# Optimization experiments

Measured on AMD Instinct MI355X. Metric: run time of the kernel, lower is better.

## Reference

```python
import jax, jax.numpy as jnp
import numpy as np

S_D, I_D, O_D = 512, 256, 256
BATCH, T = 64, 1024
SNR = 10.0  # noise scale divisor, as in sample_stable_system
SPECTRAL_RADIUS = 0.95  # stable F, mirroring sample_stable_state_matrix


def setup_inputs() -> dict:
    key = jax.random.key(0)
    ks = jax.random.split(key, 9)
    A = np.asarray(jax.random.normal(ks[0], (S_D, S_D), dtype=jnp.float32))
    F = jnp.asarray(A * (SPECTRAL_RADIUS / np.linalg.norm(A, 2)))  # scale to spectral norm 0.95
    B_mat = jax.random.normal(ks[1], (S_D, I_D), dtype=jnp.float32)
    H = jax.random.normal(ks[2], (O_D, S_D), dtype=jnp.float32)
    sqrt_S_W = jax.random.normal(ks[3], (S_D, S_D), dtype=jnp.float32) / SNR
    sqrt_S_V = jax.random.normal(ks[4], (O_D, O_D), dtype=jnp.float32) / SNR
    state = jax.random.normal(ks[5], (BATCH, S_D), dtype=jnp.float32)
    inputs = jax.random.normal(ks[6], (BATCH, T, I_D), dtype=jnp.float32)
    W_noise = jax.random.normal(ks[7], (BATCH, T, S_D), dtype=jnp.float32)
    V_noise = jax.random.normal(ks[8], (BATCH, T, O_D), dtype=jnp.float32)
    return {"state": state, "inputs": inputs, "W_noise": W_noise, "V_noise": V_noise,
            "F": F, "B_mat": B_mat, "H": H, "sqrt_S_W": sqrt_S_W, "sqrt_S_V": sqrt_S_V}


def reference(state, inputs, W_noise, V_noise, F, B_mat, H, sqrt_S_W, sqrt_S_V):
    # Process noise W = eps_W @ sqrt_S_W.T, measurement noise V = eps_V @ sqrt_S_V.T
    W = jnp.einsum('bti,ji->btj', W_noise, sqrt_S_W)          # (B, T, S_D)
    V = jnp.einsum('bti,ji->btj', V_noise, sqrt_S_V)          # (B, T, O_D)
    drive = jnp.einsum('bti,ji->btj', inputs, B_mat) + W      # u_t @ B.T + W_t

    def step(s, u):  # s_t = s_{t-1} @ F.T + u_t
        s = s @ F.T + u
        return s, s

    _, states_t = jax.lax.scan(step, state, jnp.swapaxes(drive, 0, 1))  # (T, B, S_D)
    states = jnp.swapaxes(states_t, 0, 1)                                # (B, T, S_D)
    observations = jnp.einsum('bts,os->bto', states, H) + V              # (B, T, O_D)
    return states, observations
```

## Files before the change

kernel.cpp:

```cpp
#include <hip/hip_runtime.h>
#include <hip/hip_bf16.h>


typedef short bfrag __attribute__((ext_vector_type(8)));
typedef float f32x4 __attribute__((ext_vector_type(4)));

__device__ __host__ inline unsigned short f2bf(float f) {
    union { float f; unsigned u; } x; x.f = f;
    unsigned r = x.u + 0x7fffu + ((x.u >> 16) & 1u);
    return (unsigned short)(r >> 16);
}
__device__ inline float bf2f(unsigned short h) {
    union { unsigned u; float f; } x; x.u = ((unsigned)h) << 16;
    return x.f;
}

#define MSL 262144L

struct GemmDesc {
    const void* a0; const void* a1;
    const unsigned short* b;
    float* c;
    const unsigned short* cmbeta;
    unsigned short* cm;
    unsigned short* cmT;
    long a0_base, a0_os, a0_is;
    long a1_base, a1_os, a1_is;
    long a_zq, a_zr;
    long b_base, b_ldb, b_zq, b_zr;
    long c_base, c_os, c_is, c_zq, c_zr;
    long cm_base, cmb_base, cmT_base;
    long a_shift;
    int a0_icl, a1_icl, c_icl, zdivl;
    int ksplit, K, beta;
    int a0_f32, a1_f32;
    int gxl, gyl, gz_main;
    const unsigned short* xa; const unsigned short* xb;
    unsigned short* xcm; unsigned short* xcmT;
};

__global__ __launch_bounds__(256) void gemm_k(GemmDesc d) {
    __shared__ __align__(16) unsigned short As[2][128 * 64];
    __shared__ __align__(16) unsigned short Bs[2][128 * 64];
    const int tid  = threadIdx.x;
    const int lane = tid & 63;
    const int w    = tid >> 6;
    const int wrow = (w >> 1) * 64, wcol = (w & 1) * 64;

    const unsigned nx = gridDim.x, ny = gridDim.y;
    const unsigned nwg = nx * ny * gridDim.z;
    unsigned wid = blockIdx.x + nx * (blockIdx.y + ny * blockIdx.z);
    if ((nwg & 7) == 0) wid = (wid & 7) * (nwg >> 3) + (wid >> 3);
    const int bx = wid & (nx - 1);
    const int by = (wid >> d.gxl) & (ny - 1);
    int bz = wid >> (d.gxl + d.gyl);

    if (bz >= d.gz_main) {
        if (by >= 4) return;
        const long za = (long)(bz - d.gz_main) * MSL;
        d.a0 = d.xa; d.a0_base = za; d.a0_os = 512; d.a0_is = 0; d.a0_icl = 0;
        d.a0_f32 = 0; d.a1 = nullptr;
        d.b = d.xb; d.b_base = 0; d.b_ldb = 512; d.b_zq = d.b_zr = 0;
        d.K = 512; d.ksplit = 1 << 30; d.beta = 0; d.a_shift = 0;
        d.a_zq = d.a_zr = 0;
        d.c = nullptr; d.cm = d.xcm; d.cm_base = za;
        d.c_os = 512; d.c_is = 0; d.c_icl = 0; d.c_zq = d.c_zr = 0; d.c_base = 0;
        d.cmT = d.xcmT; d.cmT_base = za;
        bz = 0;
    }
    const long zq = (long)bz >> d.zdivl;
    const long zr = (long)bz & ((1L << d.zdivl) - 1);
    const int row0 = by * 128;
    const int col0 = bx * 128;

    const int g_r = tid >> 3;
    const int g_k = (tid & 7) * 8;
    const int swz = (g_r & 7) << 3;
    const long za_ = zq * d.a_zq + zr * d.a_zr;
    const long zb_ = zq * d.b_zq + zr * d.b_zr;

    const long m0a = (1L << d.a0_icl) - 1, m1a = (1L << d.a1_icl) - 1;
    long a0off[4], a1off[4], boff[4];
#pragma unroll
    for (int i = 0; i < 4; ++i) {
        long ar = (long)row0 + i * 32 + g_r - d.a_shift;
        if (ar < 0) ar = 0;
        a0off[i] = d.a0_base + za_ + (ar >> d.a0_icl) * d.a0_os + (ar & m0a) * d.a0_is;
        a1off[i] = d.a1 ? (d.a1_base + za_ + (ar >> d.a1_icl) * d.a1_os + (ar & m1a) * d.a1_is) : 0;
        boff[i]  = d.b_base + zb_ + (long)(col0 + i * 32 + g_r) * d.b_ldb;
    }

    bfrag ar_[4], br_[4];
    auto LOADT = [&](int t) {
        const int k0 = t * 64;
        const bool s1 = (k0 >= d.ksplit);
        const int kb = (s1 ? k0 - d.ksplit : k0) + g_k;
        if (s1 ? d.a1_f32 : d.a0_f32) {
            const float* fp = (const float*)(s1 ? d.a1 : d.a0);
#pragma unroll
            for (int i = 0; i < 4; ++i) {
                const float* p = fp + (s1 ? a1off[i] : a0off[i]) + kb;
                f32x4 x0 = *(const f32x4*)p, x1 = *(const f32x4*)(p + 4);
                union { bfrag v; unsigned short h[8]; } t_;
#pragma unroll
                for (int q = 0; q < 4; ++q) { t_.h[q] = f2bf(x0[q]); t_.h[4 + q] = f2bf(x1[q]); }
                ar_[i] = t_.v;
            }
        } else {
            const unsigned short* sp = (const unsigned short*)(s1 ? d.a1 : d.a0);
#pragma unroll
            for (int i = 0; i < 4; ++i)
                ar_[i] = *(const bfrag*)(sp + (s1 ? a1off[i] : a0off[i]) + kb);
        }
#pragma unroll
        for (int i = 0; i < 4; ++i) br_[i] = *(const bfrag*)(d.b + boff[i] + k0 + g_k);
    };
    auto WRT = [&](int buf) {
#pragma unroll
        for (int i = 0; i < 4; ++i) {
            *(bfrag*)&As[buf][(i * 32 + g_r) * 64 + (g_k ^ swz)] = ar_[i];
            *(bfrag*)&Bs[buf][(i * 32 + g_r) * 64 + (g_k ^ swz)] = br_[i];
        }
    };

    f32x4 acc[4][4] = {};
    const int nt = d.K / 64;

    LOADT(0); WRT(0); __syncthreads();
    int cur = 0;
    for (int t = 0; t < nt; ++t) {
        if (t + 1 < nt) LOADT(t + 1);
#pragma unroll
        for (int ks = 0; ks < 2; ++ks) {
            const int kk = ks * 32 + (lane >> 4) * 8;
            bfrag af[4], bf_[4];
#pragma unroll
            for (int mt = 0; mt < 4; ++mt) {
                const int r = wrow + mt * 16 + (lane & 15);
                af[mt] = *(const bfrag*)&As[cur][r * 64 + (kk ^ ((r & 7) << 3))];
            }
#pragma unroll
            for (int nn = 0; nn < 4; ++nn) {
                const int r = wcol + nn * 16 + (lane & 15);
                bf_[nn] = *(const bfrag*)&Bs[cur][r * 64 + (kk ^ ((r & 7) << 3))];
            }
#pragma unroll
            for (int mt = 0; mt < 4; ++mt)
#pragma unroll
                for (int nn = 0; nn < 4; ++nn)
                    acc[mt][nn] = __builtin_amdgcn_mfma_f32_16x16x32_bf16(
                        af[mt], bf_[nn], acc[mt][nn], 0, 0, 0);
        }
        if (t + 1 < nt) WRT(cur ^ 1);
        __syncthreads();
        cur ^= 1;
    }

    const long zc = zq * d.c_zq + zr * d.c_zr;
    const long mc = (1L << d.c_icl) - 1;
#pragma unroll
    for (int mt = 0; mt < 4; ++mt) {
        const int rb = row0 + wrow + mt * 16 + ((lane >> 4) << 2);
#pragma unroll
        for (int nn = 0; nn < 4; ++nn) {
            const int cc = col0 + wcol + nn * 16 + (lane & 15);
#pragma unroll
            for (int j = 0; j < 4; ++j) {
                const long r = rb + j;
                const long off = zc + (r >> d.c_icl) * d.c_os + (r & mc) * d.c_is + cc;
                float v = (r < d.a_shift) ? 0.0f : acc[mt][nn][j];
                if (d.beta == 2) v += bf2f(d.cmbeta[d.cmb_base + off]);
                if (d.c)  d.c[d.c_base + off] = v;
                if (d.cm) d.cm[d.cm_base + off] = f2bf(v);
                if (d.cmT) d.cmT[d.cmT_base + zc + (long)cc * 512 + r] = f2bf(v);
            }
        }
    }
}

__global__ __launch_bounds__(512) void p3obs_k(
        const unsigned short* __restrict__ carry, const unsigned short* __restrict__ Gm,
        const unsigned short* __restrict__ Smir, const unsigned short* __restrict__ BopO,
        const float* __restrict__ Vn, float* __restrict__ states, float* __restrict__ obs) {
    __shared__ __align__(16) unsigned char lds[163840];
    unsigned short* As1 = (unsigned short*)(lds);
    unsigned short* Bs1 = (unsigned short*)(lds + 16384);
    unsigned short* Sb  = (unsigned short*)(lds);
    unsigned short* A2  = (unsigned short*)(lds);
    unsigned short* Ts  = (unsigned short*)(lds + 131072);

    const int tid  = threadIdx.x;
    const int lane = tid & 63;
    const int w    = tid >> 6;
    const int wm   = w >> 2, wn = w & 3;
    const int by   = blockIdx.y;
    const int k    = blockIdx.z;
    const unsigned short* G = Gm + (long)k * MSL;

    f32x4 acc[4][8] = {};

    for (int kt = 0; kt < 8; ++kt) {
        __syncthreads();
#pragma unroll
        for (int i = 0; i < 2; ++i) {
            const int fi = tid + i * 512;
            const int row = fi >> 3, kk = (fi & 7) * 8;
            const long rg = (long)by * 128 + row;
            const long c = rg >> 6, b = rg & 63;
            bfrag v = *(const bfrag*)(carry + c * 32768 + b * 512 + kt * 64 + kk);
            *(bfrag*)&As1[row * 64 + (kk ^ ((row & 7) << 3))] = v;
        }
#pragma unroll
        for (int i = 0; i < 8; ++i) {
            const int fi = tid + i * 512;
            const int row = fi >> 3, kk = (fi & 7) * 8;
            bfrag v = *(const bfrag*)(G + (long)row * 512 + kt * 64 + kk);
            *(bfrag*)&Bs1[row * 64 + (kk ^ ((row & 7) << 3))] = v;
        }
        __syncthreads();
#pragma unroll
        for (int ks = 0; ks < 2; ++ks) {
            const int kk = ks * 32 + (lane >> 4) * 8;
            bfrag af[4], bf_[8];
#pragma unroll
            for (int mt = 0; mt < 4; ++mt) {
                const int r = wm * 64 + mt * 16 + (lane & 15);
                af[mt] = *(const bfrag*)&As1[r * 64 + (kk ^ ((r & 7) << 3))];
            }
#pragma unroll
            for (int nt = 0; nt < 8; ++nt) {
                const int n = wn * 128 + nt * 16 + (lane & 15);
                bf_[nt] = *(const bfrag*)&Bs1[n * 64 + (kk ^ ((n & 7) << 3))];
            }
#pragma unroll
            for (int mt = 0; mt < 4; ++mt)
#pragma unroll
                for (int nt = 0; nt < 8; ++nt)
                    acc[mt][nt] = __builtin_amdgcn_mfma_f32_16x16x32_bf16(
                        af[mt], bf_[nt], acc[mt][nt], 0, 0, 0);
        }
    }
    __syncthreads();

#pragma unroll
    for (int mt = 0; mt < 4; ++mt) {
#pragma unroll
        for (int nt = 0; nt < 8; ++nt) {
#pragma unroll
            for (int j = 0; j < 4; ++j) {
                const int lr = wm * 64 + mt * 16 + ((lane >> 4) << 2) + j;
                const int cc = wn * 128 + nt * 16 + (lane & 15);
                const long rg = (long)by * 128 + lr;
                const long c = rg >> 6, b = rg & 63;
                const long t = c * 8 + k;
                float v = acc[mt][nt][j] + bf2f(Smir[b * 524288L + t * 512 + cc]);
                states[b * 524288L + t * 512 + cc] = v;
                Sb[lr * 512 + (cc ^ ((lr & 7) << 3))] = f2bf(v);
            }
        }
    }

    f32x4 acc2[4][4] = {};
    for (int kt = 0; kt < 12; ++kt) {
        __syncthreads();
#pragma unroll
        for (int i = 0; i < 4; ++i) {
            const int fi = tid + i * 512;
            const int row = fi >> 3, kk = (fi & 7) * 8;
            bfrag v = *(const bfrag*)(BopO + (long)row * 768 + kt * 64 + kk);
            *(bfrag*)&Ts[row * 64 + (kk ^ ((row & 7) << 3))] = v;
        }
        if (kt >= 8) {
#pragma unroll
            for (int i = 0; i < 2; ++i) {
                const int fi = tid + i * 512;
                const int row = fi >> 3, kk = (fi & 7) * 8;
                const long rg = (long)by * 128 + row;
                const long c = rg >> 6, b = rg & 63;
                const long t = c * 8 + k;
                const float* p = Vn + b * 262144L + t * 256 + (kt - 8) * 64 + kk;
                f32x4 x0 = *(const f32x4*)p, x1 = *(const f32x4*)(p + 4);
                union { bfrag v; unsigned short h[8]; } u;
#pragma unroll
                for (int q = 0; q < 4; ++q) { u.h[q] = f2bf(x0[q]); u.h[4 + q] = f2bf(x1[q]); }
                *(bfrag*)&A2[row * 64 + (kk ^ ((row & 7) << 3))] = u.v;
            }
        }
        __syncthreads();
#pragma unroll
        for (int ks = 0; ks < 2; ++ks) {
            const int kk = ks * 32 + (lane >> 4) * 8;
            bfrag af[4], bf_[4];
#pragma unroll
            for (int mt = 0; mt < 4; ++mt) {
                const int r = wm * 64 + mt * 16 + (lane & 15);
                af[mt] = (kt < 8)
                    ? *(const bfrag*)&Sb[r * 512 + ((kt * 64 + kk) ^ ((r & 7) << 3))]
                    : *(const bfrag*)&A2[r * 64 + (kk ^ ((r & 7) << 3))];
            }
#pragma unroll
            for (int nt = 0; nt < 4; ++nt) {
                const int n = wn * 64 + nt * 16 + (lane & 15);
                bf_[nt] = *(const bfrag*)&Ts[n * 64 + (kk ^ ((n & 7) << 3))];
            }
#pragma unroll
            for (int mt = 0; mt < 4; ++mt)
#pragma unroll
                for (int nt = 0; nt < 4; ++nt)
                    acc2[mt][nt] = __builtin_amdgcn_mfma_f32_16x16x32_bf16(
                        af[mt], bf_[nt], acc2[mt][nt], 0, 0, 0);
        }
    }
#pragma unroll
    for (int mt = 0; mt < 4; ++mt) {
#pragma unroll
        for (int nt = 0; nt < 4; ++nt) {
#pragma unroll
            for (int j = 0; j < 4; ++j) {
                const int lr = wm * 64 + mt * 16 + ((lane >> 4) << 2) + j;
                const int cc = wn * 64 + nt * 16 + (lane & 15);
                const long rg = (long)by * 128 + lr;
                const long c = rg >> 6, b = rg & 63;
                const long t = c * 8 + k;
                obs[b * 262144L + t * 256 + cc] = acc2[mt][nt][j];
            }
        }
    }
}

__global__ void cvt_k(const float* src, unsigned short* dst, long n) {
    long i = ((long)blockIdx.x * 256 + threadIdx.x) * 8;
    const long stride = (long)gridDim.x * 256 * 8;
    for (; i < n; i += stride) {
        f32x4 x0 = *(const f32x4*)(src + i), x1 = *(const f32x4*)(src + i + 4);
        union { bfrag v; unsigned short h[8]; } t;
#pragma unroll
        for (int q = 0; q < 4; ++q) { t.h[q] = f2bf(x0[q]); t.h[4 + q] = f2bf(x1[q]); }
        *(bfrag*)(dst + i) = t.v;
    }
}

__global__ void build_ops_k(const float* F, const float* Bm, const float* H,
                            const float* sW, const float* sV,
                            unsigned short* bopd, unsigned short* bopo,
                            unsigned short* G1, unsigned short* Gt1) {
    int i = blockIdx.x * 256 + threadIdx.x;
    const int n1 = 512 * 768, n2 = 256 * 768, n3 = 512 * 512;
    if (i < n1) { int n = i / 768, k = i % 768;
        bopd[i] = f2bf(k < 256 ? Bm[n * 256 + k] : sW[n * 512 + (k - 256)]); return; }
    i -= n1;
    if (i < n2) { int o = i / 768, k = i % 768;
        bopo[i] = f2bf(k < 512 ? H[o * 512 + k] : sV[o * 256 + (k - 512)]); return; }
    i -= n2;
    if (i < n3) { G1[i] = f2bf(F[i]); return; }
    i -= n3;
    if (i < n3) { int r = i / 512, c = i % 512; Gt1[i] = f2bf(F[c * 512 + r]); }
}

__global__ void init_carry_k(const float* st0, const unsigned short* Smir,
                             unsigned short* dst) {
    const long i8 = ((long)blockIdx.x * 256 + threadIdx.x) * 8;
    if (i8 >= 4194304L) return;
    const long c = i8 >> 15, rem = i8 & 32767L;
    const long b = rem >> 9, s = rem & 511L;
    union { bfrag v; unsigned short h[8]; } t;
    if (c == 0) {
        const float* p = st0 + b * 512 + s;
        f32x4 x0 = *(const f32x4*)p, x1 = *(const f32x4*)(p + 4);
#pragma unroll
        for (int q = 0; q < 4; ++q) { t.h[q] = f2bf(x0[q]); t.h[4 + q] = f2bf(x1[q]); }
    } else {
        t.v = *(const bfrag*)(Smir + b * 524288L + (c - 1) * 4096L + 3584L + s);
    }
    *(bfrag*)(dst + i8) = t.v;
}

static GemmDesc D0() {
    GemmDesc d = {};
    d.zdivl = 30;
    d.ksplit = 1 << 30;
    d.b_ldb = 512; d.K = 512;
    d.gz_main = 1 << 30;
    return d;
}

extern "C" void kernel_launch(void* const* d_in, const int* in_sizes, int n_in,
                              void* d_out, int out_size, void* d_ws, size_t ws_size,
                              hipStream_t stream) {
    const float* st0 = (const float*)d_in[0];
    const float* inp = (const float*)d_in[1];
    const float* Wn  = (const float*)d_in[2];
    const float* Vn  = (const float*)d_in[3];
    const float* F   = (const float*)d_in[4];
    const float* Bm  = (const float*)d_in[5];
    const float* H   = (const float*)d_in[6];
    const float* sW  = (const float*)d_in[7];
    const float* sV  = (const float*)d_in[8];

    float* states = (float*)d_out;
    float* obs    = states + 33554432L;

    const long MS = MSL;
    const long CB = 32768;
    const int  NC = 128;
    const int  CL = 8;
    const long TOS = 524288;
    const long COS = (long)CL * 512;

    unsigned short* inpb = (unsigned short*)states;
    unsigned short* Wnb  = inpb + 16777216L;

    unsigned short* Smir = (unsigned short*)d_ws;
    unsigned short* G    = Smir + 33554432L;
    unsigned short* Gt   = G + 8 * MS;
    unsigned short* Qb   = Gt + 8 * MS;
    unsigned short* Qtb  = Qb + 6 * MS;
    unsigned short* BopD = Qtb + 6 * MS;
    unsigned short* BopO = BopD + 512 * 768;
    unsigned short* a0m  = BopO + 256 * 768;
    unsigned short* a1m  = a0m + (long)NC * CB;
    (void)in_sizes; (void)n_in; (void)out_size; (void)ws_size;

    auto L = [&](const GemmDesc& d, int gx, int gxl, int gy, int gyl, int gz) {
        GemmDesc dd = d; dd.gxl = gxl; dd.gyl = gyl;
        gemm_k<<<dim3(gx, gy, gz), dim3(256), 0, stream>>>(dd);
    };

    cvt_k<<<dim3(2048), dim3(256), 0, stream>>>(inp, inpb, 16777216L);
    cvt_k<<<dim3(2048), dim3(256), 0, stream>>>(Wn, Wnb, 33554432L);

    build_ops_k<<<dim3(4352), dim3(256), 0, stream>>>(F, Bm, H, sW, sV, BopD, BopO, G, Gt);

    {
        GemmDesc d = D0();
        d.a0 = inpb; d.a0_os = 256;
        d.a1 = Wnb;  d.a1_os = 512;
        d.ksplit = 256; d.K = 768;
        d.b = BopD; d.b_ldb = 768;
        d.cm = Smir; d.c_os = 512;
        L(d, 4, 2, 512, 9, 1);
    }

    for (int k = 1; k < CL; ++k) {
        GemmDesc d = D0();
        d.a0 = Smir; d.a0_base = (long)(k - 1) * 512;
        d.a0_icl = 7; d.a0_is = COS; d.a0_os = TOS;
        d.b = G;
        d.c_base = (long)k * 512;
        d.c_icl = 7; d.c_is = COS; d.c_os = TOS;
        d.beta = 2; d.cmbeta = Smir; d.cmb_base = (long)k * 512;
        d.cm = Smir; d.cm_base = (long)k * 512;
        d.gz_main = 1;
        int n;
        if (k == 1)      { d.xa = G;           d.xb = Gt;           d.xcm = G + MS;      d.xcmT = Gt + MS;      n = 1; }
        else if (k == 2) { d.xa = G;           d.xb = Gt + MS;      d.xcm = G + 2 * MS;  d.xcmT = Gt + 2 * MS;  n = 2; }
        else if (k == 3) { d.xa = G;           d.xb = Gt + 3 * MS;  d.xcm = G + 4 * MS;  d.xcmT = Gt + 4 * MS;  n = 4; }
        else if (k == 4) { d.xa = G + 7 * MS;  d.xb = Gt + 7 * MS;  d.xcm = Qb;          d.xcmT = Qtb;          n = 1; }
        else             { int j = k - 5;
                           d.xa = Qb + j * MS; d.xb = Qtb + j * MS; d.xcm = Qb + (j+1)*MS; d.xcmT = Qtb + (j+1)*MS; n = 1; }
        L(d, 4, 2, 64, 6, 1 + n);
    }

    init_carry_k<<<dim3(2048), dim3(256), 0, stream>>>(st0, Smir, a0m);

    unsigned short* curm = a0m;
    unsigned short* nxtm = a1m;
    for (int s = 1; s < NC; s <<= 1) {
        GemmDesc d = D0();
        d.a0 = curm; d.a0_os = 512;
        d.a_shift = (long)s * 64;
        if (s == 1) { d.b = G;  d.b_base = 7 * MS; }
        else        { d.b = Qb; d.b_base = (long)(__builtin_ctz(s) - 1) * MS; }
        d.beta = 2; d.cmbeta = curm; d.cmb_base = 0;
        d.cm = nxtm; d.c_os = 512;
        int n = 0;
        if (s == 1) { d.gz_main = 1; d.xa = Qb + 3 * MS; d.xb = Qtb + 3 * MS;
                      d.xcm = Qb + 4 * MS; d.xcmT = Qtb + 4 * MS; n = 1; }
        if (s == 2) { d.gz_main = 1; d.xa = Qb + 4 * MS; d.xb = Qtb + 4 * MS;
                      d.xcm = Qb + 5 * MS; d.xcmT = nullptr; n = 1; }
        L(d, 4, 2, 64, 6, 1 + n);
        unsigned short* tm = curm; curm = nxtm; nxtm = tm;
    }

    p3obs_k<<<dim3(1, 64, 8), dim3(512), 0, stream>>>(
        curm, G, Smir, BopO, Vn, states, obs);
}
```

Before: 703.7 us.

## Restructure intra-chunk scan into log-depth passes and double-buffer observation kernel

Replaces the seven sequential intra-chunk propagation GEMMs with three doubling passes (shifts 1, 2, 4). Each pass uses ping-pong buffers plus auxiliary copy blocks, and the G-power computations are folded into existing launches, including the first drive GEMM. The observation kernel gets register-staged double-buffered LDS loads to overlap global loads with MFMA, and its grid is reordered so the chunk index is on x. The f32 A-path is removed from the GEMM. The goal is fewer serialized launches and less load latency, at the cost of more total GEMM work and extra copy traffic through the states buffer.

Result: slower. 940.6 us (+33.7%).

```diff
diff --git a/kernel.cpp b/kernel.cpp
--- a/kernel.cpp
+++ b/kernel.cpp
@@ -18,12 +18,13 @@
 #define MSL 262144L
 
 struct GemmDesc {
-    const void* a0; const void* a1;
+    const unsigned short* a0;
     const unsigned short* b;
     float* c;
     const unsigned short* cmbeta;
     unsigned short* cm;
     unsigned short* cmT;
+    const unsigned short* a1;
     long a0_base, a0_os, a0_is;
     long a1_base, a1_os, a1_is;
     long a_zq, a_zr;
@@ -33,8 +34,8 @@
     long a_shift;
     int a0_icl, a1_icl, c_icl, zdivl;
     int ksplit, K, beta;
-    int a0_f32, a1_f32;
-    int gxl, gyl, gz_main;
+    int gxl, gyl, gz_main, gz_ncp;
+    const unsigned short* cp_src; unsigned short* cp_dst; long cp_nrows;
     const unsigned short* xa; const unsigned short* xb;
     unsigned short* xcm; unsigned short* xcmT;
 };
@@ -56,10 +57,22 @@
     int bz = wid >> (d.gxl + d.gyl);
 
     if (bz >= d.gz_main) {
+        const int aux_z = bz - d.gz_main - d.gz_ncp;
+        if (aux_z < 0) {
+            const long total = (long)nx * ny * 256;
+            const long flatb = wid & (nx * ny - 1);
+            for (long i8 = (flatb * 256 + tid) * 8; i8 < d.cp_nrows * 512; i8 += total * 8) {
+                const long r = i8 >> 9, s = i8 & 511;
+                const long t = r >> 13, q = r & 8191;
+                const long off = (q >> 7) * 524288L + (q & 127) * 4096L + t * 512L + s;
+                *(bfrag*)(d.cp_dst + off) = *(const bfrag*)(d.cp_src + off);
+            }
+            return;
+        }
         if (by >= 4) return;
-        const long za = (long)(bz - d.gz_main) * MSL;
+        const long za = (long)aux_z * MSL;
         d.a0 = d.xa; d.a0_base = za; d.a0_os = 512; d.a0_is = 0; d.a0_icl = 0;
-        d.a0_f32 = 0; d.a1 = nullptr;
+        d.a1 = nullptr;
         d.b = d.xb; d.b_base = 0; d.b_ldb = 512; d.b_zq = d.b_zr = 0;
         d.K = 512; d.ksplit = 1 << 30; d.beta = 0; d.a_shift = 0;
         d.a_zq = d.a_zr = 0;
@@ -95,23 +108,10 @@
         const int k0 = t * 64;
         const bool s1 = (k0 >= d.ksplit);
         const int kb = (s1 ? k0 - d.ksplit : k0) + g_k;
-        if (s1 ? d.a1_f32 : d.a0_f32) {
-            const float* fp = (const float*)(s1 ? d.a1 : d.a0);
-#pragma unroll
-            for (int i = 0; i < 4; ++i) {
-                const float* p = fp + (s1 ? a1off[i] : a0off[i]) + kb;
-                f32x4 x0 = *(const f32x4*)p, x1 = *(const f32x4*)(p + 4);
-                union { bfrag v; unsigned short h[8]; } t_;
-#pragma unroll
-                for (int q = 0; q < 4; ++q) { t_.h[q] = f2bf(x0[q]); t_.h[4 + q] = f2bf(x1[q]); }
-                ar_[i] = t_.v;
-            }
-        } else {
-            const unsigned short* sp = (const unsigned short*)(s1 ? d.a1 : d.a0);
-#pragma unroll
-            for (int i = 0; i < 4; ++i)
-                ar_[i] = *(const bfrag*)(sp + (s1 ? a1off[i] : a0off[i]) + kb);
-        }
+        const unsigned short* sp = s1 ? d.a1 : d.a0;
+#pragma unroll
+        for (int i = 0; i < 4; ++i)
+            ar_[i] = *(const bfrag*)(sp + (s1 ? a1off[i] : a0off[i]) + kb);
 #pragma unroll
         for (int i = 0; i < 4; ++i) br_[i] = *(const bfrag*)(d.b + boff[i] + k0 + g_k);
     };
@@ -183,41 +183,54 @@
         const unsigned short* __restrict__ Smir, const unsigned short* __restrict__ BopO,
         const float* __restrict__ Vn, float* __restrict__ states, float* __restrict__ obs) {
     __shared__ __align__(16) unsigned char lds[163840];
-    unsigned short* As1 = (unsigned short*)(lds);
-    unsigned short* Bs1 = (unsigned short*)(lds + 16384);
-    unsigned short* Sb  = (unsigned short*)(lds);
-    unsigned short* A2  = (unsigned short*)(lds);
-    unsigned short* Ts  = (unsigned short*)(lds + 131072);
+#define BS1(buf) ((unsigned short*)(lds + (buf) * 65536))
+#define AS1(buf) ((unsigned short*)(lds + 131072 + (buf) * 16384))
+    unsigned short* Sb = (unsigned short*)lds;
+    unsigned short* Ts = (unsigned short*)(lds + 131072);
+    unsigned short* A2 = (unsigned short*)lds;
 
     const int tid  = threadIdx.x;
     const int lane = tid & 63;
     const int w    = tid >> 6;
     const int wm   = w >> 2, wn = w & 3;
+    const int k    = blockIdx.x;
     const int by   = blockIdx.y;
-    const int k    = blockIdx.z;
     const unsigned short* G = Gm + (long)k * MSL;
 
+    const int srow = tid >> 3;
+    const int skk  = (tid & 7) * 8;
+    const int sw   = (srow & 7) << 3;
+
+    bfrag areg[2], breg[8];
+    auto LOADT = [&](int kt) {
+#pragma unroll
+        for (int i = 0; i < 2; ++i) {
+            const int row = srow + i * 64;
+            const long rg = (long)by * 128 + row;
+            areg[i] = *(const bfrag*)(carry + (rg >> 6) * 32768 + (rg & 63) * 512 + kt * 64 + skk);
+        }
+#pragma unroll
+        for (int i = 0; i < 8; ++i)
+            breg[i] = *(const bfrag*)(G + (long)(srow + i * 64) * 512 + kt * 64 + skk);
+    };
+    auto WRT = [&](int buf) {
+        unsigned short* as = AS1(buf);
+        unsigned short* bs = BS1(buf);
+#pragma unroll
+        for (int i = 0; i < 2; ++i)
+            *(bfrag*)&as[(srow + i * 64) * 64 + (skk ^ sw)] = areg[i];
+#pragma unroll
+        for (int i = 0; i < 8; ++i)
+            *(bfrag*)&bs[(srow + i * 64) * 64 + (skk ^ sw)] = breg[i];
+    };
+
     f32x4 acc[4][8] = {};
-
+    LOADT(0); WRT(0); __syncthreads();
+    int cur = 0;
     for (int kt = 0; kt < 8; ++kt) {
-        __syncthreads();
-#pragma unroll
-        for (int i = 0; i < 2; ++i) {
-            const int fi = tid + i * 512;
-            const int row = fi >> 3, kk = (fi & 7) * 8;
-            const long rg = (long)by * 128 + row;
-            const long c = rg >> 6, b = rg & 63;
-            bfrag v = *(const bfrag*)(carry + c * 32768 + b * 512 + kt * 64 + kk);
-            *(bfrag*)&As1[row * 64 + (kk ^ ((row & 7) << 3))] = v;
-        }
-#pragma unroll
-        for (int i = 0; i < 8; ++i) {
-            const int fi = tid + i * 512;
-            const int row = fi >> 3, kk = (fi & 7) * 8;
-            bfrag v = *(const bfrag*)(G + (long)row * 512 + kt * 64 + kk);
-            *(bfrag*)&Bs1[row * 64 + (kk ^ ((row & 7) << 3))] = v;
-        }
-        __syncthreads();
+        if (kt < 7) LOADT(kt + 1);
+        const unsigned short* as = AS1(cur);
+        const unsigned short* bs = BS1(cur);
 #pragma unroll
         for (int ks = 0; ks < 2; ++ks) {
             const int kk = ks * 32 + (lane >> 4) * 8;
@@ -225,12 +238,12 @@
 #pragma unroll
             for (int mt = 0; mt < 4; ++mt) {
                 const int r = wm * 64 + mt * 16 + (lane & 15);
-                af[mt] = *(const bfrag*)&As1[r * 64 + (kk ^ ((r & 7) << 3))];
+                af[mt] = *(const bfrag*)&as[r * 64 + (kk ^ ((r & 7) << 3))];
             }
 #pragma unroll
             for (int nt = 0; nt < 8; ++nt) {
                 const int n = wn * 128 + nt * 16 + (lane & 15);
-                bf_[nt] = *(const bfrag*)&Bs1[n * 64 + (kk ^ ((n & 7) << 3))];
+                bf_[nt] = *(const bfrag*)&bs[n * 64 + (kk ^ ((n & 7) << 3))];
             }
 #pragma unroll
             for (int mt = 0; mt < 4; ++mt)
@@ -239,8 +252,10 @@
                     acc[mt][nt] = __builtin_amdgcn_mfma_f32_16x16x32_bf16(
                         af[mt], bf_[nt], acc[mt][nt], 0, 0, 0);
         }
-    }
-    __syncthreads();
+        if (kt < 7) WRT(cur ^ 1);
+        __syncthreads();
+        cur ^= 1;
+    }
 
 #pragma unroll
     for (int mt = 0; mt < 4; ++mt) {
@@ -251,8 +266,8 @@
                 const int lr = wm * 64 + mt * 16 + ((lane >> 4) << 2) + j;
                 const int cc = wn * 128 + nt * 16 + (lane & 15);
                 const long rg = (long)by * 128 + lr;
-                const long c = rg >> 6, b = rg & 63;
-                const long t = c * 8 + k;
+                const long b = rg & 63;
+                const long t = (rg >> 6) * 8 + k;
                 float v = acc[mt][nt][j] + bf2f(Smir[b * 524288L + t * 512 + cc]);
                 states[b * 524288L + t * 512 + cc] = v;
                 Sb[lr * 512 + (cc ^ ((lr & 7) << 3))] = f2bf(v);
@@ -276,8 +291,8 @@
                 const int fi = tid + i * 512;
                 const int row = fi >> 3, kk = (fi & 7) * 8;
                 const long rg = (long)by * 128 + row;
-                const long c = rg >> 6, b = rg & 63;
-                const long t = c * 8 + k;
+                const long b = rg & 63;
+                const long t = (rg >> 6) * 8 + k;
                 const float* p = Vn + b * 262144L + t * 256 + (kt - 8) * 64 + kk;
                 f32x4 x0 = *(const f32x4*)p, x1 = *(const f32x4*)(p + 4);
                 union { bfrag v; unsigned short h[8]; } u;
@@ -320,12 +335,14 @@
                 const int lr = wm * 64 + mt * 16 + ((lane >> 4) << 2) + j;
                 const int cc = wn * 64 + nt * 16 + (lane & 15);
                 const long rg = (long)by * 128 + lr;
-                const long c = rg >> 6, b = rg & 63;
-                const long t = c * 8 + k;
+                const long b = rg & 63;
+                const long t = (rg >> 6) * 8 + k;
                 obs[b * 262144L + t * 256 + cc] = acc2[mt][nt][j];
             }
         }
     }
+#undef BS1
+#undef AS1
 }
 
 __global__ void cvt_k(const float* src, unsigned short* dst, long n) {
@@ -403,12 +420,12 @@
     const long MS = MSL;
     const long CB = 32768;
     const int  NC = 128;
-    const int  CL = 8;
     const long TOS = 524288;
-    const long COS = (long)CL * 512;
+    const long COS = 4096;
 
     unsigned short* inpb = (unsigned short*)states;
     unsigned short* Wnb  = inpb + 16777216L;
+    unsigned short* BufA = (unsigned short*)states;
 
     unsigned short* Smir = (unsigned short*)d_ws;
     unsigned short* G    = Smir + 33554432L;
@@ -438,50 +455,72 @@
         d.ksplit = 256; d.K = 768;
         d.b = BopD; d.b_ldb = 768;
         d.cm = Smir; d.c_os = 512;
-        L(d, 4, 2, 512, 9, 1);
-    }
-
-    for (int k = 1; k < CL; ++k) {
+        d.gz_main = 1;
+        d.xa = G; d.xb = Gt; d.xcm = G + MS; d.xcmT = Gt + MS;
+        L(d, 4, 2, 512, 9, 2);
+    }
+
+    {
         GemmDesc d = D0();
-        d.a0 = Smir; d.a0_base = (long)(k - 1) * 512;
-        d.a0_icl = 7; d.a0_is = COS; d.a0_os = TOS;
+        d.a0 = Smir; d.a0_icl = 7; d.a0_os = TOS; d.a0_is = COS; d.a_zr = 512;
         d.b = G;
-        d.c_base = (long)k * 512;
-        d.c_icl = 7; d.c_is = COS; d.c_os = TOS;
-        d.beta = 2; d.cmbeta = Smir; d.cmb_base = (long)k * 512;
-        d.cm = Smir; d.cm_base = (long)k * 512;
-        d.gz_main = 1;
-        int n;
-        if (k == 1)      { d.xa = G;           d.xb = Gt;           d.xcm = G + MS;      d.xcmT = Gt + MS;      n = 1; }
-        else if (k == 2) { d.xa = G;           d.xb = Gt + MS;      d.xcm = G + 2 * MS;  d.xcmT = Gt + 2 * MS;  n = 2; }
-        else if (k == 3) { d.xa = G;           d.xb = Gt + 3 * MS;  d.xcm = G + 4 * MS;  d.xcmT = Gt + 4 * MS;  n = 4; }
-        else if (k == 4) { d.xa = G + 7 * MS;  d.xb = Gt + 7 * MS;  d.xcm = Qb;          d.xcmT = Qtb;          n = 1; }
-        else             { int j = k - 5;
-                           d.xa = Qb + j * MS; d.xb = Qtb + j * MS; d.xcm = Qb + (j+1)*MS; d.xcmT = Qtb + (j+1)*MS; n = 1; }
-        L(d, 4, 2, 64, 6, 1 + n);
+        d.cm = BufA; d.cm_base = 512;
+        d.c_icl = 7; d.c_os = TOS; d.c_is = COS; d.c_zr = 512;
+        d.beta = 2; d.cmbeta = Smir; d.cmb_base = 512;
+        d.gz_main = 7; d.gz_ncp = 1;
+        d.cp_src = Smir; d.cp_dst = BufA; d.cp_nrows = 8192;
+        d.xa = G; d.xb = Gt + MS; d.xcm = G + 2 * MS; d.xcmT = Gt + 2 * MS;
+        L(d, 4, 2, 64, 6, 10);
+    }
+    {
+        GemmDesc d = D0();
+        d.a0 = BufA; d.a0_icl = 7; d.a0_os = TOS; d.a0_is = COS; d.a_zr = 512;
+        d.b = G + MS;
+        d.cm = Smir; d.cm_base = 1024;
+        d.c_icl = 7; d.c_os = TOS; d.c_is = COS; d.c_zr = 512;
+        d.beta = 2; d.cmbeta = BufA; d.cmb_base = 1024;
+        d.gz_main = 6; d.gz_ncp = 1;
+        d.cp_src = BufA; d.cp_dst = Smir; d.cp_nrows = 16384;
+        d.xa = G; d.xb = Gt + 3 * MS; d.xcm = G + 4 * MS; d.xcmT = Gt + 4 * MS;
+        L(d, 4, 2, 64, 6, 11);
+    }
+    {
+        GemmDesc d = D0();
+        d.a0 = Smir; d.a0_icl = 7; d.a0_os = TOS; d.a0_is = COS; d.a_zr = 512;
+        d.b = G + 3 * MS;
+        d.cm = Smir; d.cm_base = 2048;
+        d.c_icl = 7; d.c_os = TOS; d.c_is = COS; d.c_zr = 512;
+        d.beta = 2; d.cmbeta = Smir; d.cmb_base = 2048;
+        d.gz_main = 4;
+        d.xa = G + 7 * MS; d.xb = Gt + 7 * MS; d.xcm = Qb; d.xcmT = Qtb;
+        L(d, 4, 2, 64, 6, 5);
     }
 
     init_carry_k<<<dim3(2048), dim3(256), 0, stream>>>(st0, Smir, a0m);
 
     unsigned short* curm = a0m;
     unsigned short* nxtm = a1m;
-    for (int s = 1; s < NC; s <<= 1) {
+    int ksi = 0;
+    for (int s = 1; s < NC; s <<= 1, ++ksi) {
         GemmDesc d = D0();
         d.a0 = curm; d.a0_os = 512;
         d.a_shift = (long)s * 64;
-        if (s == 1) { d.b = G;  d.b_base = 7 * MS; }
-        else        { d.b = Qb; d.b_base = (long)(__builtin_ctz(s) - 1) * MS; }
+        if (s == 1) { d.b = G + 7 * MS; }
+        else        { d.b = Qb + (long)(__builtin_ctz(s) - 1) * MS; }
         d.beta = 2; d.cmbeta = curm; d.cmb_base = 0;
         d.cm = nxtm; d.c_os = 512;
         int n = 0;
-        if (s == 1) { d.gz_main = 1; d.xa = Qb + 3 * MS; d.xb = Qtb + 3 * MS;
-                      d.xcm = Qb + 4 * MS; d.xcmT = Qtb + 4 * MS; n = 1; }
-        if (s == 2) { d.gz_main = 1; d.xa = Qb + 4 * MS; d.xb = Qtb + 4 * MS;
-                      d.xcm = Qb + 5 * MS; d.xcmT = nullptr; n = 1; }
+        if (ksi < 5) {
+            d.gz_main = 1;
+            d.xa = Qb + (long)ksi * MS; d.xb = Qtb + (long)ksi * MS;
+            d.xcm = Qb + (long)(ksi + 1) * MS;
+            d.xcmT = (ksi < 4) ? (Qtb + (long)(ksi + 1) * MS) : nullptr;
+            n = 1;
+        }
         L(d, 4, 2, 64, 6, 1 + n);
         unsigned short* tm = curm; curm = nxtm; nxtm = tm;
     }
 
-    p3obs_k<<<dim3(1, 64, 8), dim3(512), 0, stream>>>(
+    p3obs_k<<<dim3(8, 64, 1), dim3(512), 0, stream>>>(
         curm, G, Smir, BopO, Vn, states, obs);
 }
```

## Halve chunk length to four steps and double chunk count in scan

Applied to the files above, without the earlier changes.

Changes the chunked linear recurrence from 128 chunks of 8 steps to 256 chunks of 4 steps, reducing the number of sequential intra-chunk GEMM launches. The inter-chunk doubling scan gains an extra level over twice as many rows, and F-power precomputation is folded into the first drive GEMM launch. It also drops the unused fp32 A-load path from the GEMM kernel. This trades serial launch depth against more total work in the carry-propagation scan.

After: 867.9 us. 1.23x slower.

```diff
diff --git a/kernel.cpp b/kernel.cpp
--- a/kernel.cpp
+++ b/kernel.cpp
@@ -18,7 +18,7 @@
 #define MSL 262144L
 
 struct GemmDesc {
-    const void* a0; const void* a1;
+    const unsigned short* a0; const unsigned short* a1;
     const unsigned short* b;
     float* c;
     const unsigned short* cmbeta;
@@ -33,7 +33,6 @@
     long a_shift;
     int a0_icl, a1_icl, c_icl, zdivl;
     int ksplit, K, beta;
-    int a0_f32, a1_f32;
     int gxl, gyl, gz_main;
     const unsigned short* xa; const unsigned short* xb;
     unsigned short* xcm; unsigned short* xcmT;
@@ -59,7 +58,7 @@
         if (by >= 4) return;
         const long za = (long)(bz - d.gz_main) * MSL;
         d.a0 = d.xa; d.a0_base = za; d.a0_os = 512; d.a0_is = 0; d.a0_icl = 0;
-        d.a0_f32 = 0; d.a1 = nullptr;
+        d.a1 = nullptr;
         d.b = d.xb; d.b_base = 0; d.b_ldb = 512; d.b_zq = d.b_zr = 0;
         d.K = 512; d.ksplit = 1 << 30; d.beta = 0; d.a_shift = 0;
         d.a_zq = d.a_zr = 0;
@@ -95,23 +94,10 @@
         const int k0 = t * 64;
         const bool s1 = (k0 >= d.ksplit);
         const int kb = (s1 ? k0 - d.ksplit : k0) + g_k;
-        if (s1 ? d.a1_f32 : d.a0_f32) {
-            const float* fp = (const float*)(s1 ? d.a1 : d.a0);
-#pragma unroll
-            for (int i = 0; i < 4; ++i) {
-                const float* p = fp + (s1 ? a1off[i] : a0off[i]) + kb;
-                f32x4 x0 = *(const f32x4*)p, x1 = *(const f32x4*)(p + 4);
-                union { bfrag v; unsigned short h[8]; } t_;
-#pragma unroll
-                for (int q = 0; q < 4; ++q) { t_.h[q] = f2bf(x0[q]); t_.h[4 + q] = f2bf(x1[q]); }
-                ar_[i] = t_.v;
-            }
-        } else {
-            const unsigned short* sp = (const unsigned short*)(s1 ? d.a1 : d.a0);
-#pragma unroll
-            for (int i = 0; i < 4; ++i)
-                ar_[i] = *(const bfrag*)(sp + (s1 ? a1off[i] : a0off[i]) + kb);
-        }
+        const unsigned short* sp = s1 ? d.a1 : d.a0;
+#pragma unroll
+        for (int i = 0; i < 4; ++i)
+            ar_[i] = *(const bfrag*)(sp + (s1 ? a1off[i] : a0off[i]) + kb);
 #pragma unroll
         for (int i = 0; i < 4; ++i) br_[i] = *(const bfrag*)(d.b + boff[i] + k0 + g_k);
     };
@@ -252,7 +238,7 @@
                 const int cc = wn * 128 + nt * 16 + (lane & 15);
                 const long rg = (long)by * 128 + lr;
                 const long c = rg >> 6, b = rg & 63;
-                const long t = c * 8 + k;
+                const long t = c * 4 + k;
                 float v = acc[mt][nt][j] + bf2f(Smir[b * 524288L + t * 512 + cc]);
                 states[b * 524288L + t * 512 + cc] = v;
                 Sb[lr * 512 + (cc ^ ((lr & 7) << 3))] = f2bf(v);
@@ -277,7 +263,7 @@
                 const int row = fi >> 3, kk = (fi & 7) * 8;
                 const long rg = (long)by * 128 + row;
                 const long c = rg >> 6, b = rg & 63;
-                const long t = c * 8 + k;
+                const long t = c * 4 + k;
                 const float* p = Vn + b * 262144L + t * 256 + (kt - 8) * 64 + kk;
                 f32x4 x0 = *(const f32x4*)p, x1 = *(const f32x4*)(p + 4);
                 union { bfrag v; unsigned short h[8]; } u;
@@ -321,7 +307,7 @@
                 const int cc = wn * 64 + nt * 16 + (lane & 15);
                 const long rg = (long)by * 128 + lr;
                 const long c = rg >> 6, b = rg & 63;
-                const long t = c * 8 + k;
+                const long t = c * 4 + k;
                 obs[b * 262144L + t * 256 + cc] = acc2[mt][nt][j];
             }
         }
@@ -360,7 +346,7 @@
 __global__ void init_carry_k(const float* st0, const unsigned short* Smir,
                              unsigned short* dst) {
     const long i8 = ((long)blockIdx.x * 256 + threadIdx.x) * 8;
-    if (i8 >= 4194304L) return;
+    if (i8 >= 8388608L) return;
     const long c = i8 >> 15, rem = i8 & 32767L;
     const long b = rem >> 9, s = rem & 511L;
     union { bfrag v; unsigned short h[8]; } t;
@@ -370,7 +356,7 @@
 #pragma unroll
         for (int q = 0; q < 4; ++q) { t.h[q] = f2bf(x0[q]); t.h[4 + q] = f2bf(x1[q]); }
     } else {
-        t.v = *(const bfrag*)(Smir + b * 524288L + (c - 1) * 4096L + 3584L + s);
+        t.v = *(const bfrag*)(Smir + b * 524288L + (c - 1) * 2048L + 1536L + s);
     }
     *(bfrag*)(dst + i8) = t.v;
 }
@@ -402,8 +388,8 @@
 
     const long MS = MSL;
     const long CB = 32768;
-    const int  NC = 128;
-    const int  CL = 8;
+    const int  NC = 256;
+    const int  CL = 4;
     const long TOS = 524288;
     const long COS = (long)CL * 512;
 
@@ -412,9 +398,9 @@
 
     unsigned short* Smir = (unsigned short*)d_ws;
     unsigned short* G    = Smir + 33554432L;
-    unsigned short* Gt   = G + 8 * MS;
-    unsigned short* Qb   = Gt + 8 * MS;
-    unsigned short* Qtb  = Qb + 6 * MS;
+    unsigned short* Gt   = G + 4 * MS;
+    unsigned short* Qb   = Gt + 4 * MS;
+    unsigned short* Qtb  = Qb + 7 * MS;
     unsigned short* BopD = Qtb + 6 * MS;
     unsigned short* BopO = BopD + 512 * 768;
     unsigned short* a0m  = BopO + 256 * 768;
@@ -438,50 +424,53 @@
         d.ksplit = 256; d.K = 768;
         d.b = BopD; d.b_ldb = 768;
         d.cm = Smir; d.c_os = 512;
-        L(d, 4, 2, 512, 9, 1);
+        d.gz_main = 1;
+        d.xa = G; d.xb = Gt; d.xcm = G + MS; d.xcmT = Gt + MS;
+        L(d, 4, 2, 512, 9, 2);
     }
 
     for (int k = 1; k < CL; ++k) {
         GemmDesc d = D0();
         d.a0 = Smir; d.a0_base = (long)(k - 1) * 512;
-        d.a0_icl = 7; d.a0_is = COS; d.a0_os = TOS;
+        d.a0_icl = 8; d.a0_is = COS; d.a0_os = TOS;
         d.b = G;
         d.c_base = (long)k * 512;
-        d.c_icl = 7; d.c_is = COS; d.c_os = TOS;
+        d.c_icl = 8; d.c_is = COS; d.c_os = TOS;
         d.beta = 2; d.cmbeta = Smir; d.cmb_base = (long)k * 512;
         d.cm = Smir; d.cm_base = (long)k * 512;
         d.gz_main = 1;
         int n;
-        if (k == 1)      { d.xa = G;           d.xb = Gt;           d.xcm = G + MS;      d.xcmT = Gt + MS;      n = 1; }
-        else if (k == 2) { d.xa = G;           d.xb = Gt + MS;      d.xcm = G + 2 * MS;  d.xcmT = Gt + 2 * MS;  n = 2; }
-        else if (k == 3) { d.xa = G;           d.xb = Gt + 3 * MS;  d.xcm = G + 4 * MS;  d.xcmT = Gt + 4 * MS;  n = 4; }
-        else if (k == 4) { d.xa = G + 7 * MS;  d.xb = Gt + 7 * MS;  d.xcm = Qb;          d.xcmT = Qtb;          n = 1; }
-        else             { int j = k - 5;
-                           d.xa = Qb + j * MS; d.xb = Qtb + j * MS; d.xcm = Qb + (j+1)*MS; d.xcmT = Qtb + (j+1)*MS; n = 1; }
-        L(d, 4, 2, 64, 6, 1 + n);
-    }
-
-    init_carry_k<<<dim3(2048), dim3(256), 0, stream>>>(st0, Smir, a0m);
+        if (k == 1)      { d.xa = G;          d.xb = Gt + MS;     d.xcm = G + 2 * MS; d.xcmT = Gt + 2 * MS; n = 2; }
+        else if (k == 2) { d.xa = G + 3 * MS; d.xb = Gt + 3 * MS; d.xcm = Qb;         d.xcmT = Qtb;         n = 1; }
+        else             { d.xa = Qb;         d.xb = Qtb;         d.xcm = Qb + MS;    d.xcmT = Qtb + MS;    n = 1; }
+        L(d, 4, 2, 128, 7, 1 + n);
+    }
+
+    init_carry_k<<<dim3(4096), dim3(256), 0, stream>>>(st0, Smir, a0m);
 
     unsigned short* curm = a0m;
     unsigned short* nxtm = a1m;
-    for (int s = 1; s < NC; s <<= 1) {
+    int ri = 0;
+    for (int s = 1; s < NC; s <<= 1, ++ri) {
         GemmDesc d = D0();
         d.a0 = curm; d.a0_os = 512;
         d.a_shift = (long)s * 64;
-        if (s == 1) { d.b = G;  d.b_base = 7 * MS; }
-        else        { d.b = Qb; d.b_base = (long)(__builtin_ctz(s) - 1) * MS; }
+        if (s == 1) { d.b = G + 3 * MS; }
+        else        { d.b = Qb + (long)(__builtin_ctz(s) - 1) * MS; }
         d.beta = 2; d.cmbeta = curm; d.cmb_base = 0;
         d.cm = nxtm; d.c_os = 512;
         int n = 0;
-        if (s == 1) { d.gz_main = 1; d.xa = Qb + 3 * MS; d.xb = Qtb + 3 * MS;
-                      d.xcm = Qb + 4 * MS; d.xcmT = Qtb + 4 * MS; n = 1; }
-        if (s == 2) { d.gz_main = 1; d.xa = Qb + 4 * MS; d.xb = Qtb + 4 * MS;
-                      d.xcm = Qb + 5 * MS; d.xcmT = nullptr; n = 1; }
-        L(d, 4, 2, 64, 6, 1 + n);
+        if (ri < 5) {
+            d.gz_main = 1;
+            d.xa = Qb + (long)(ri + 1) * MS; d.xb = Qtb + (long)(ri + 1) * MS;
+            d.xcm = Qb + (long)(ri + 2) * MS;
+            d.xcmT = (ri < 4) ? (Qtb + (long)(ri + 2) * MS) : nullptr;
+            n = 1;
+        }
+        L(d, 4, 2, 128, 7, 1 + n);
         unsigned short* tm = curm; curm = nxtm; nxtm = tm;
     }
 
-    p3obs_k<<<dim3(1, 64, 8), dim3(512), 0, stream>>>(
+    p3obs_k<<<dim3(1, 128, 4), dim3(512), 0, stream>>>(
         curm, G, Smir, BopO, Vn, states, obs);
 }
```

## Replace intra-chunk scan GEMM launches with a persistent LDS-resident scan kernel

Applied to the files above, without the earlier changes.

Replaces the seven per-step intra-chunk GEMM launches with a single scan_k kernel. Each block keeps 32 chunk rows of the state in LDS and streams F tiles through double-buffered LDS for all 7 sequential steps. The power-of-F matrix products are regrouped: F^2, F^3 and F^4..F^7 are computed in separate small launches, and the later Q powers are folded into the carry-propagation rounds. This cuts launch count and global round trips of the state, but each scan block re-reads F from global memory for every step. The scan also runs on only 256 blocks, so occupancy is limited. The dead fp32 A-load path is removed from the GEMM kernel.

Result: slower. 828.0 us (+17.7%).

```diff
diff --git a/kernel.cpp b/kernel.cpp
--- a/kernel.cpp
+++ b/kernel.cpp
@@ -18,7 +18,7 @@
 #define MSL 262144L
 
 struct GemmDesc {
-    const void* a0; const void* a1;
+    const unsigned short* a0; const unsigned short* a1;
     const unsigned short* b;
     float* c;
     const unsigned short* cmbeta;
@@ -33,7 +33,6 @@
     long a_shift;
     int a0_icl, a1_icl, c_icl, zdivl;
     int ksplit, K, beta;
-    int a0_f32, a1_f32;
     int gxl, gyl, gz_main;
     const unsigned short* xa; const unsigned short* xb;
     unsigned short* xcm; unsigned short* xcmT;
@@ -59,7 +58,7 @@
         if (by >= 4) return;
         const long za = (long)(bz - d.gz_main) * MSL;
         d.a0 = d.xa; d.a0_base = za; d.a0_os = 512; d.a0_is = 0; d.a0_icl = 0;
-        d.a0_f32 = 0; d.a1 = nullptr;
+        d.a1 = nullptr;
         d.b = d.xb; d.b_base = 0; d.b_ldb = 512; d.b_zq = d.b_zr = 0;
         d.K = 512; d.ksplit = 1 << 30; d.beta = 0; d.a_shift = 0;
         d.a_zq = d.a_zr = 0;
@@ -95,23 +94,10 @@
         const int k0 = t * 64;
         const bool s1 = (k0 >= d.ksplit);
         const int kb = (s1 ? k0 - d.ksplit : k0) + g_k;
-        if (s1 ? d.a1_f32 : d.a0_f32) {
-            const float* fp = (const float*)(s1 ? d.a1 : d.a0);
-#pragma unroll
-            for (int i = 0; i < 4; ++i) {
-                const float* p = fp + (s1 ? a1off[i] : a0off[i]) + kb;
-                f32x4 x0 = *(const f32x4*)p, x1 = *(const f32x4*)(p + 4);
-                union { bfrag v; unsigned short h[8]; } t_;
-#pragma unroll
-                for (int q = 0; q < 4; ++q) { t_.h[q] = f2bf(x0[q]); t_.h[4 + q] = f2bf(x1[q]); }
-                ar_[i] = t_.v;
-            }
-        } else {
-            const unsigned short* sp = (const unsigned short*)(s1 ? d.a1 : d.a0);
-#pragma unroll
-            for (int i = 0; i < 4; ++i)
-                ar_[i] = *(const bfrag*)(sp + (s1 ? a1off[i] : a0off[i]) + kb);
-        }
+        const unsigned short* sp = s1 ? d.a1 : d.a0;
+#pragma unroll
+        for (int i = 0; i < 4; ++i)
+            ar_[i] = *(const bfrag*)(sp + (s1 ? a1off[i] : a0off[i]) + kb);
 #pragma unroll
         for (int i = 0; i < 4; ++i) br_[i] = *(const bfrag*)(d.b + boff[i] + k0 + g_k);
     };
@@ -175,6 +161,101 @@
                 if (d.cmT) d.cmT[d.cmT_base + zc + (long)cc * 512 + r] = f2bf(v);
             }
         }
+    }
+}
+
+__global__ __launch_bounds__(512) void scan_k(
+        unsigned short* __restrict__ Smir, const unsigned short* __restrict__ Fm) {
+    __shared__ __align__(16) unsigned char lds[163840];
+    unsigned short* Scur = (unsigned short*)lds;
+
+    const int tid  = threadIdx.x;
+    const int lane = tid & 63;
+    const int w    = tid >> 6;
+    const long rg0 = (long)blockIdx.x * 32;
+
+    const int fr = tid >> 3;
+    const int fk = (tid & 7) * 8;
+
+    bfrag freg[8];
+    auto LOADF = [&](int kt) {
+#pragma unroll
+        for (int i = 0; i < 8; ++i)
+            freg[i] = *(const bfrag*)(Fm + (long)(fr + i * 64) * 512 + kt * 64 + fk);
+    };
+    auto WRTF = [&](int buf) {
+        unsigned short* Fs = (unsigned short*)(lds + 32768 + buf * 65536);
+#pragma unroll
+        for (int i = 0; i < 8; ++i) {
+            const int r = fr + i * 64;
+            *(bfrag*)&Fs[r * 64 + (fk ^ ((r & 7) << 3))] = freg[i];
+        }
+    };
+
+#pragma unroll
+    for (int i = 0; i < 4; ++i) {
+        const int fi = tid + i * 512;
+        const int row = fi >> 6;
+        const int col = (fi & 63) * 8;
+        const long rg = rg0 + row;
+        const long b = rg >> 7, c = rg & 127;
+        bfrag v = *(const bfrag*)(Smir + b * 524288L + c * 4096L + col);
+        *(bfrag*)&Scur[row * 512 + (col ^ ((row & 7) << 3))] = v;
+    }
+    LOADF(0); WRTF(0);
+    __syncthreads();
+
+    int cur = 0;
+    for (int t = 1; t < 8; ++t) {
+        f32x4 acc[2][4] = {};
+        for (int kt = 0; kt < 8; ++kt) {
+            const bool pre = !(t == 7 && kt == 7);
+            if (pre) LOADF((kt + 1) & 7);
+            const unsigned short* Fs = (const unsigned short*)(lds + 32768 + cur * 65536);
+#pragma unroll
+            for (int ks = 0; ks < 2; ++ks) {
+                const int kk = ks * 32 + (lane >> 4) * 8;
+                bfrag af[2], bf_[4];
+#pragma unroll
+                for (int mt = 0; mt < 2; ++mt) {
+                    const int r = mt * 16 + (lane & 15);
+                    const int col = kt * 64 + kk;
+                    af[mt] = *(const bfrag*)&Scur[r * 512 + (col ^ ((r & 7) << 3))];
+                }
+#pragma unroll
+                for (int nt = 0; nt < 4; ++nt) {
+                    const int n = w * 64 + nt * 16 + (lane & 15);
+                    bf_[nt] = *(const bfrag*)&Fs[n * 64 + (kk ^ ((n & 7) << 3))];
+                }
+#pragma unroll
+                for (int mt = 0; mt < 2; ++mt)
+#pragma unroll
+                    for (int nt = 0; nt < 4; ++nt)
+                        acc[mt][nt] = __builtin_amdgcn_mfma_f32_16x16x32_bf16(
+                            af[mt], bf_[nt], acc[mt][nt], 0, 0, 0);
+            }
+            if (pre) WRTF(cur ^ 1);
+            __syncthreads();
+            cur ^= 1;
+        }
+#pragma unroll
+        for (int mt = 0; mt < 2; ++mt) {
+#pragma unroll
+            for (int nt = 0; nt < 4; ++nt) {
+#pragma unroll
+                for (int j = 0; j < 4; ++j) {
+                    const int lr = mt * 16 + ((lane >> 4) << 2) + j;
+                    const int cc = w * 64 + nt * 16 + (lane & 15);
+                    const long rg = rg0 + lr;
+                    const long b = rg >> 7, c = rg & 127;
+                    const long off = b * 524288L + c * 4096L + (long)t * 512 + cc;
+                    const unsigned short bv = f2bf(acc[mt][nt][j] + bf2f(Smir[off]));
+                    Smir[off] = bv;
+                    Scur[lr * 512 + (cc ^ ((lr & 7) << 3))] = bv;
+                }
+            }
+        }
+        __syncthreads();
     }
 }
 
@@ -403,9 +484,6 @@
     const long MS = MSL;
     const long CB = 32768;
     const int  NC = 128;
-    const int  CL = 8;
-    const long TOS = 524288;
-    const long COS = (long)CL * 512;
 
     unsigned short* inpb = (unsigned short*)states;
     unsigned short* Wnb  = inpb + 16777216L;
@@ -438,46 +516,48 @@
         d.ksplit = 256; d.K = 768;
         d.b = BopD; d.b_ldb = 768;
         d.cm = Smir; d.c_os = 512;
-        L(d, 4, 2, 512, 9, 1);
-    }
-
-    for (int k = 1; k < CL; ++k) {
+        d.gz_main = 1;
+        d.xa = G; d.xb = Gt; d.xcm = G + MS; d.xcmT = Gt + MS;
+        L(d, 4, 2, 512, 9, 2);
+    }
+
+    {
         GemmDesc d = D0();
-        d.a0 = Smir; d.a0_base = (long)(k - 1) * 512;
-        d.a0_icl = 7; d.a0_is = COS; d.a0_os = TOS;
-        d.b = G;
-        d.c_base = (long)k * 512;
-        d.c_icl = 7; d.c_is = COS; d.c_os = TOS;
-        d.beta = 2; d.cmbeta = Smir; d.cmb_base = (long)k * 512;
-        d.cm = Smir; d.cm_base = (long)k * 512;
-        d.gz_main = 1;
-        int n;
-        if (k == 1)      { d.xa = G;           d.xb = Gt;           d.xcm = G + MS;      d.xcmT = Gt + MS;      n = 1; }
-        else if (k == 2) { d.xa = G;           d.xb = Gt + MS;      d.xcm = G + 2 * MS;  d.xcmT = Gt + 2 * MS;  n = 2; }
-        else if (k == 3) { d.xa = G;           d.xb = Gt + 3 * MS;  d.xcm = G + 4 * MS;  d.xcmT = Gt + 4 * MS;  n = 4; }
-        else if (k == 4) { d.xa = G + 7 * MS;  d.xb = Gt + 7 * MS;  d.xcm = Qb;          d.xcmT = Qtb;          n = 1; }
-        else             { int j = k - 5;
-                           d.xa = Qb + j * MS; d.xb = Qtb + j * MS; d.xcm = Qb + (j+1)*MS; d.xcmT = Qtb + (j+1)*MS; n = 1; }
-        L(d, 4, 2, 64, 6, 1 + n);
-    }
+        d.gz_main = 0;
+        d.xa = G; d.xb = Gt + MS; d.xcm = G + 2 * MS; d.xcmT = Gt + 2 * MS;
+        L(d, 4, 2, 4, 2, 2);
+    }
+    {
+        GemmDesc d = D0();
+        d.gz_main = 0;
+        d.xa = G; d.xb = Gt + 3 * MS; d.xcm = G + 4 * MS; d.xcmT = Gt + 4 * MS;
+        L(d, 4, 2, 4, 2, 4);
+    }
+
+    scan_k<<<dim3(256), dim3(512), 0, stream>>>(Smir, G);
 
     init_carry_k<<<dim3(2048), dim3(256), 0, stream>>>(st0, Smir, a0m);
 
     unsigned short* curm = a0m;
     unsigned short* nxtm = a1m;
-    for (int s = 1; s < NC; s <<= 1) {
+    int ri = 0;
+    for (int s = 1; s < NC; s <<= 1, ++ri) {
         GemmDesc d = D0();
         d.a0 = curm; d.a0_os = 512;
         d.a_shift = (long)s * 64;
-        if (s == 1) { d.b = G;  d.b_base = 7 * MS; }
-        else        { d.b = Qb; d.b_base = (long)(__builtin_ctz(s) - 1) * MS; }
+        if (s == 1) { d.b = G + 7 * MS; }
+        else        { d.b = Qb + (long)(__builtin_ctz(s) - 1) * MS; }
         d.beta = 2; d.cmbeta = curm; d.cmb_base = 0;
         d.cm = nxtm; d.c_os = 512;
         int n = 0;
-        if (s == 1) { d.gz_main = 1; d.xa = Qb + 3 * MS; d.xb = Qtb + 3 * MS;
-                      d.xcm = Qb + 4 * MS; d.xcmT = Qtb + 4 * MS; n = 1; }
-        if (s == 2) { d.gz_main = 1; d.xa = Qb + 4 * MS; d.xb = Qtb + 4 * MS;
-                      d.xcm = Qb + 5 * MS; d.xcmT = nullptr; n = 1; }
+        if (ri < 6) {
+            d.gz_main = 1;
+            d.xa = ri ? (Qb + (long)(ri - 1) * MS) : (G + 7 * MS);
+            d.xb = ri ? (Qtb + (long)(ri - 1) * MS) : (Gt + 7 * MS);
+            d.xcm = Qb + (long)ri * MS;
+            d.xcmT = (ri < 5) ? (Qtb + (long)ri * MS) : nullptr;
+            n = 1;
+        }
         L(d, 4, 2, 64, 6, 1 + n);
         unsigned short* tm = curm; curm = nxtm; nxtm = tm;
     }
```
